# Optimization experiments

Hardware: AMD Instinct MI355X
Metric: run time of the kernel (lower is better)

The kernel has to match this reference:

```python
import jax, jax.numpy as jnp
import numpy as np

B, N, D = 4, 2048, 1024
H = 8
DK = D // H            # 128, head qk dim (pre feature map)
DV = D // H            # 128, head v dim
DF = 2 * DK            # 256, hedgehog feature dim
CHUNK = 64
RMS_EPS = 1e-5


def setup_inputs() -> dict:
    key = jax.random.key(0)
    ks = jax.random.split(key, 10)
    s = D ** -0.5
    x = jax.random.normal(ks[0], (B, N, D), dtype=jnp.float32)
    Wq = jax.random.normal(ks[1], (D, D), dtype=jnp.float32) * s
    Wk = jax.random.normal(ks[2], (D, D), dtype=jnp.float32) * s
    Wv = jax.random.normal(ks[3], (D, D), dtype=jnp.float32) * s
    Wo = jax.random.normal(ks[4], (D, D), dtype=jnp.float32) * s
    eye = jnp.eye(DK, dtype=jnp.float32)
    # Hedgehog maps are initialized as identity; add small noise to exercise math
    fmq_w = eye + 0.02 * jax.random.normal(ks[5], (DK, DK), dtype=jnp.float32)
    fmq_b = 0.02 * jax.random.normal(ks[6], (DK,), dtype=jnp.float32)
    fmk_w = eye + 0.02 * jax.random.normal(ks[7], (DK, DK), dtype=jnp.float32)
    fmk_b = 0.02 * jax.random.normal(ks[8], (DK,), dtype=jnp.float32)
    rms_w = 1.0 + 0.1 * jax.random.normal(ks[9], (DV,), dtype=jnp.float32)
    return {"x": x, "Wq": Wq, "Wk": Wk, "Wv": Wv, "Wo": Wo,
            "fmq_w": fmq_w, "fmq_b": fmq_b, "fmk_w": fmk_w, "fmk_b": fmk_b,
            "rms_w": rms_w}


def _hedgehog(x, w, b):
    # x: [B,H,N,DK]; Linear then concat(exp(y), exp(-y)) -> [B,H,N,2*DK]
    y = jnp.einsum('bhnd,ed->bhne', x, w) + b
    return jnp.concatenate([jnp.exp(y), jnp.exp(-y)], axis=-1)


def _fused_chunk_linear_attn(q, k, v):
    # Causal linear attention via chunked recurrence.
    # q,k: [B,H,N,DF]; v: [B,H,N,DV]; q already scaled.
    b, h, n, df = q.shape
    dv = v.shape[-1]
    nc = n // CHUNK
    def to_chunks(t):
        d = t.shape[-1]
        return t.reshape(b, h, nc, CHUNK, d).transpose(2, 0, 1, 3, 4)  # [Nc,B,H,C,d]
    qc, kc, vc = to_chunks(q), to_chunks(k), to_chunks(v)
    mask = jnp.tril(jnp.ones((CHUNK, CHUNK), dtype=bool))

    def step(S, inp):
        qi, ki, vi = inp                                   # [B,H,C,*]
        attn = jnp.einsum('bhcd,bhed->bhce', qi, ki)       # intra-chunk scores
        attn = jnp.where(mask, attn, 0.0)                  # causal (inclusive)
        intra = jnp.einsum('bhce,bhev->bhcv', attn, vi)
        inter = jnp.einsum('bhcd,bhdv->bhcv', qi, S)       # past-chunk state
        S = S + jnp.einsum('bhcd,bhcv->bhdv', ki, vi)
        return S, intra + inter

    S0 = jnp.zeros((b, h, df, dv), dtype=q.dtype)
    _, oc = jax.lax.scan(step, S0, (qc, kc, vc))           # oc: [Nc,B,H,C,DV]
    return oc.transpose(1, 2, 0, 3, 4).reshape(b, h, n, dv)


def reference(x, Wq, Wk, Wv, Wo, fmq_w, fmq_b, fmk_w, fmk_b, rms_w):
    b, n, d = x.shape
    split = lambda t: t.reshape(b, n, H, -1).transpose(0, 2, 1, 3)  # b h n d
    q = split(x @ Wq.T)
    k = split(x @ Wk.T)
    v = split(x @ Wv.T)
    q = _hedgehog(q, fmq_w, fmq_b)          # [B,H,N,DF]
    k = _hedgehog(k, fmk_w, fmk_b)
    scale = q.shape[-1] ** -0.5             # fla default: feat_dim**-0.5
    o = _fused_chunk_linear_attn(q * scale, k, v)
    # RMSNorm over head_v_dim
    o = o * jax.lax.rsqrt(jnp.mean(o * o, axis=-1, keepdims=True) + RMS_EPS) * rms_w
    o = o.transpose(0, 2, 1, 3).reshape(b, n, H * DV)
    return o @ Wo.T
```

## Files before the change

### kernel.cpp

```cpp
#include <hip/hip_runtime.h>
#include <cstdint>
#include <cstddef>

#define DEV __device__ __forceinline__

typedef __attribute__((ext_vector_type(8))) short   short8;
typedef __attribute__((ext_vector_type(4))) short   sshort4;
typedef __attribute__((ext_vector_type(8))) __bf16  bf16x8;
typedef __attribute__((ext_vector_type(4))) float   f32x4;

typedef void as1_void __attribute__((address_space(1)));
typedef void as3_void __attribute__((address_space(3)));

DEV short f2b(float f) {
  unsigned u = __float_as_uint(f);
  unsigned r = (u + 0x7fffu + ((u >> 16) & 1u)) >> 16;
  return (short)r;
}
DEV float b2f(short s) {
  return __uint_as_float(((unsigned)(unsigned short)s) << 16);
}

DEV void gload16(const void* g, void* l) {
  __builtin_amdgcn_global_load_lds((as1_void*)g, (as3_void*)l, 16, 0, 0);
}

DEV bf16x8 ld8(const short* p) { return *reinterpret_cast<const bf16x8*>(p); }

DEV f32x4 mfma16(bf16x8 a, bf16x8 b, f32x4 c) {
  return __builtin_amdgcn_mfma_f32_16x16x32_bf16(a, b, c, 0, 0, 0);
}

__global__ void prep_kernel(const float* __restrict__ x, const float* __restrict__ Wo,
                            const float* __restrict__ Wq, const float* __restrict__ Wk,
                            const float* __restrict__ Wv,
                            const float* __restrict__ fmq_w, const float* __restrict__ fmk_w,
                            short* __restrict__ x_b, short* __restrict__ Wo_b,
                            short* __restrict__ Wcat)
{
  const int blk = blockIdx.x;
  const int tid = threadIdx.x;
  if (blk < 5120) {
    const float* src;
    short* dst;
    int i;
    if (blk < 4096)      { src = x;  dst = x_b;            i = (blk * 256 + tid) * 8; }
    else if (blk < 4608) { src = Wo; dst = Wo_b;           i = ((blk - 4096) * 256 + tid) * 8; }
    else                 { src = Wv; dst = Wcat + 2097152; i = ((blk - 4608) * 256 + tid) * 8; }
    float4 a = *(const float4*)(src + i);
    float4 b = *(const float4*)(src + i + 4);
    short8 o;
    o[0] = f2b(a.x); o[1] = f2b(a.y); o[2] = f2b(a.z); o[3] = f2b(a.w);
    o[4] = f2b(b.x); o[5] = f2b(b.y); o[6] = f2b(b.z); o[7] = f2b(b.w);
    *(short8*)(dst + i) = o;
  } else {
    __shared__ float fm[16 * 128];
    const int eb = blk - 5120;
    const int sel = eb >> 6, h = (eb >> 3) & 7, eg = eb & 7;
    const float* W   = sel ? Wk : Wq;
    const float* fmw = sel ? fmk_w : fmq_w;
    const int e0 = eg * 16;
    for (int i = tid; i < 2048; i += 256) fm[i] = fmw[e0 * 128 + i];
    __syncthreads();
    float acc[16][4] = {};
    for (int d = 0; d < 128; d += 4) {
      f32x4 w0 = *(const f32x4*)(W + (size_t)(h * 128 + d + 0) * 1024 + tid * 4);
      f32x4 w1 = *(const f32x4*)(W + (size_t)(h * 128 + d + 1) * 1024 + tid * 4);
      f32x4 w2 = *(const f32x4*)(W + (size_t)(h * 128 + d + 2) * 1024 + tid * 4);
      f32x4 w3 = *(const f32x4*)(W + (size_t)(h * 128 + d + 3) * 1024 + tid * 4);
#pragma unroll
      for (int e = 0; e < 16; ++e) {
        f32x4 fv = *(const f32x4*)&fm[e * 128 + d];
#pragma unroll
        for (int c = 0; c < 4; ++c)
          acc[e][c] += fv[0] * w0[c] + fv[1] * w1[c] + fv[2] * w2[c] + fv[3] * w3[c];
      }
    }
#pragma unroll
    for (int e = 0; e < 16; ++e) {
      sshort4 o;
#pragma unroll
      for (int c = 0; c < 4; ++c) o[c] = f2b(acc[e][c]);
      *(sshort4*)(Wcat + (size_t)(sel * 1024 + h * 128 + e0 + e) * 1024 + tid * 4) = o;
    }
  }
}

template<int EPI>
__launch_bounds__(512, 2)
__global__ void gemm256(const short* __restrict__ A, const short* __restrict__ B,
                        const int K, const int N, float* __restrict__ C,
                        const float* __restrict__ qb, const float* __restrict__ kb,
                        short* __restrict__ qf, short* __restrict__ kf,
                        short* __restrict__ kfT, short* __restrict__ vT)
{
  __shared__ __align__(16) short lds[65536];
  float* ep = (float*)lds;

  const int tid = threadIdx.x;
  const int w = tid >> 6, l = tid & 63;
  const int wr = w >> 2, wc = w & 3;

  const int nbx = gridDim.x;
  const int orig = blockIdx.y * nbx + blockIdx.x;
  const int cpx = (nbx * gridDim.y) >> 3;
  const int wg = (orig & 7) * cpx + (orig >> 3);
  const int m0 = (wg / nbx) * 256, n0 = (wg % nbx) * 256;

  const int srow = tid >> 3;
  const int scol = ((tid & 7) ^ (srow & 7)) * 8;
  const int wbase = w * 8;

  f32x4 acc[8][4] = {};
  bf16x8 af[4][2];
  bf16x8 bg[2][2][2];

  auto STG = [&](const short* src, int g0, int p, int aoff, int R, int t) {
    gload16(src + (size_t)(g0 + R + srow) * K + t * 64 + scol,
            lds + p * 32768 + aoff + (R + wbase) * 64);
  };

#pragma unroll
  for (int R = 0; R < 256; R += 64) {
    STG(A, m0, 0, 0, R, 0);
    STG(B, n0, 0, 16384, R, 0);
    STG(A, m0, 1, 0, R, 1);
    STG(B, n0, 1, 16384, R, 1);
  }
  asm volatile("s_waitcnt vmcnt(0)" ::: "memory");
  __builtin_amdgcn_s_barrier();

#define PHASE(p, q, DOLDA, DOLDB, STAGES, TAIL) { \
    if (DOLDA) { \
      _Pragma("unroll") \
      for (int m = 0; m < 4; ++m) { \
        const int r = wr * 128 + ((q) >> 1) * 64 + m * 16 + (l & 15); \
        _Pragma("unroll") \
        for (int kk = 0; kk < 2; ++kk) \
          af[m][kk] = ld8(lds + (p) * 32768 + r * 64 + ((kk * 4 + (l >> 4)) ^ (r & 7)) * 8); \
      } \
    } \
    if (DOLDB) { \
      _Pragma("unroll") \
      for (int n = 0; n < 2; ++n) { \
        const int r = wc * 64 + ((q) & 1) * 32 + n * 16 + (l & 15); \
        _Pragma("unroll") \
        for (int kk = 0; kk < 2; ++kk) \
          bg[(q) & 1][n][kk] = ld8(lds + (p) * 32768 + 16384 + r * 64 + ((kk * 4 + (l >> 4)) ^ (r & 7)) * 8); \
      } \
    } \
    STAGES; \
    __builtin_amdgcn_s_barrier(); \
    asm volatile("s_waitcnt lgkmcnt(0)" ::: "memory"); \
    __builtin_amdgcn_sched_barrier(0); \
    __builtin_amdgcn_s_setprio(1); \
    _Pragma("unroll") \
    for (int m = 0; m < 4; ++m) \
      _Pragma("unroll") \
      for (int n = 0; n < 2; ++n) \
        _Pragma("unroll") \
        for (int kk = 0; kk < 2; ++kk) \
          acc[((q) >> 1) * 4 + m][((q) & 1) * 2 + n] = \
            mfma16(af[m][kk], bg[(q) & 1][n][kk], acc[((q) >> 1) * 4 + m][((q) & 1) * 2 + n]); \
    __builtin_amdgcn_s_setprio(0); \
    TAIL; \
    __builtin_amdgcn_s_barrier(); \
  }

  const int NI = K >> 7;
  for (int i = 0; i < NI; ++i) {
    const int t1 = 2 * i + 1, t2 = 2 * i + 2, t3 = 2 * i + 3;
    const bool sE = (i < NI - 1), sL = (i > 0);
    PHASE(0, 0, 1, 1, {
      if (sL) { STG(A, m0, 1, 0, 64, t1); STG(A, m0, 1, 0, 192, t1);
                STG(B, n0, 1, 16384, 0, t1); STG(B, n0, 1, 16384, 64, t1); } }, {});
    PHASE(0, 1, 0, 1, {
      if (sL) { STG(B, n0, 1, 16384, 128, t1); STG(B, n0, 1, 16384, 192, t1); } }, {});
    PHASE(0, 2, 1, 0, {
      if (sE) { STG(A, m0, 0, 0, 0, t2); STG(A, m0, 0, 0, 128, t2); } }, {});
    PHASE(0, 3, 0, 0, {}, {
      if (i == NI - 1) { asm volatile("s_waitcnt vmcnt(0)" ::: "memory"); }
      else             { asm volatile("s_waitcnt vmcnt(2)" ::: "memory"); } });
    PHASE(1, 0, 1, 1, {
      if (sE) { STG(A, m0, 0, 0, 64, t2); STG(A, m0, 0, 0, 192, t2); } }, {});
    PHASE(1, 1, 0, 1, {
      if (sE) { STG(B, n0, 0, 16384, 0, t2); STG(B, n0, 0, 16384, 64, t2); } }, {});
    PHASE(1, 2, 1, 0, {
      if (sE) { STG(B, n0, 0, 16384, 128, t2); STG(B, n0, 0, 16384, 192, t2); } }, {});
    PHASE(1, 3, 0, 0, {
      if (sE) { STG(A, m0, 1, 0, 0, t3); STG(A, m0, 1, 0, 128, t3); } }, {
      asm volatile("s_waitcnt vmcnt(2)" ::: "memory"); });
  }
#undef PHASE

  const int seg = (EPI == 1) ? (n0 >> 10) : 0;
  const int b = m0 >> 11, tok0 = m0 & 2047, c0 = tok0 >> 6;
  const int hbase = (n0 & 1023) >> 7;
  const int bh0 = b * 8 + hbase;

#pragma unroll
  for (int h = 0; h < 4; ++h) {
    __syncthreads();
    if (wr == (h >> 1)) {
      const int mbase = (h & 1) * 4;
#pragma unroll
      for (int n = 0; n < 4; ++n) {
        const int cl = wc * 64 + n * 16 + (l & 15);
        float bb = 0.f;
        if constexpr (EPI == 1) bb = (seg == 0) ? qb[cl & 127] : (seg == 1) ? kb[cl & 127] : 0.f;
#pragma unroll
        for (int m4 = 0; m4 < 4; ++m4)
#pragma unroll
          for (int r = 0; r < 4; ++r) {
            const int rl = m4 * 16 + (l >> 4) * 4 + r;
            ep[rl * 264 + (cl ^ ((rl & 3) << 2))] = acc[mbase + m4][n][r] + bb;
          }
      }
    }
    __syncthreads();

    if constexpr (EPI == 0) {
#pragma unroll
      for (int it = 0; it < 8; ++it) {
        const int tl = it * 8 + (tid >> 6);
        const int cc4 = (tid & 63) * 4;
        f32x4 v4 = *(const f32x4*)&ep[tl * 264 + (cc4 ^ ((tl & 3) << 2))];
        *(f32x4*)(C + (size_t)(m0 + h * 64 + tl) * N + n0 + cc4) = v4;
      }
    } else {
      const int cc = c0 + h;
      if (seg <= 1) {
        short* dst = (seg == 0) ? qf : kf;
        const float sc = (seg == 0) ? 0.0625f : 1.0f;
#pragma unroll
        for (int it = 0; it < 8; ++it) {
          const int tl = it * 8 + (tid >> 6);
          const int cc4 = (tid & 63) * 4;
          f32x4 y4 = *(const f32x4*)&ep[tl * 264 + (cc4 ^ ((tl & 3) << 2))];
          sshort4 sp, sm;
#pragma unroll
          for (int j = 0; j < 4; ++j) {
            sp[j] = f2b(__expf(y4[j]) * sc);
            sm[j] = f2b(__expf(-y4[j]) * sc);
          }
          const int hh = cc4 >> 7, e = cc4 & 127;
          short* rowp = dst + ((size_t)(bh0 + hh) * 2048 + tok0 + h * 64 + tl) * 256;
          *(sshort4*)(rowp + e)       = sp;
          *(sshort4*)(rowp + 128 + e) = sm;
        }
        if (seg == 1) {
#pragma unroll
          for (int p2 = 0; p2 < 8; ++p2) {
            const int idx = p2 * 512 + tid;
            const int er = idx >> 3, oct = (idx & 7) * 8;
            const int hh = er >> 8, rr = er & 255, e = rr & 127, sg = rr >> 7;
            const int cgc = hh * 128 + e;
            short8 o;
#pragma unroll
            for (int ii = 0; ii < 8; ++ii) {
              float y = ep[(oct + ii) * 264 + (cgc ^ (((oct + ii) & 3) << 2))];
              o[ii] = f2b(__expf(sg ? -y : y));
            }
            *(short8*)(kfT + ((size_t)(bh0 + hh) * 32 + cc) * 16384 + (size_t)rr * 64 + oct) = o;
          }
        }
      } else {
#pragma unroll
        for (int p2 = 0; p2 < 4; ++p2) {
          const int idx = p2 * 512 + tid;
          const int er = idx >> 3, oct = (idx & 7) * 8;
          const int hh = er >> 7, vv = er & 127;
          short8 o;
#pragma unroll
          for (int ii = 0; ii < 8; ++ii)
            o[ii] = f2b(ep[(oct + ii) * 264 + (er ^ (((oct + ii) & 3) << 2))]);
          *(short8*)(vT + ((size_t)(bh0 + hh) * 32 + cc) * 8192 + (size_t)vv * 64 + oct) = o;
        }
      }
    }
  }
}

__launch_bounds__(256, 3)
__global__ void passA_kernel(const short* __restrict__ kfT, const short* __restrict__ vT,
                             short* __restrict__ GT)
{
  const int bhc = blockIdx.x;
  const int tid = threadIdx.x, w = tid >> 6, l = tid & 63;
  __shared__ __align__(16) short skT[256 * 64];
  __shared__ __align__(16) short svt[128 * 64];
  const short* kg = kfT + (size_t)bhc * 256 * 64;
  const short* vg = vT  + (size_t)bhc * 128 * 64;
  short* G = GT + (size_t)bhc * 128 * 256;
  const int sr8 = l >> 3, sl8 = ((l & 7) ^ sr8) * 8;

#pragma unroll
  for (int j = 0; j < 8; ++j) {
    const int seg = w * 8 + j;
    gload16(kg + (size_t)(seg * 8 + sr8) * 64 + sl8, skT + seg * 512);
  }
#pragma unroll
  for (int j = 0; j < 4; ++j) {
    const int seg = w * 4 + j;
    gload16(vg + (size_t)(seg * 8 + sr8) * 64 + sl8, svt + seg * 512);
  }
  __syncthreads();

#pragma unroll
  for (int mi = 0; mi < 2; ++mi) {
    const int v0 = w * 32 + mi * 16;
    bf16x8 a[2];
#pragma unroll
    for (int ks = 0; ks < 2; ++ks)
      a[ks] = ld8(svt + (v0 + (l & 15)) * 64 + ((ks * 4 + (l >> 4)) ^ (l & 7)) * 8);
    f32x4 acc[16] = {};
#pragma unroll
    for (int nt = 0; nt < 16; ++nt)
#pragma unroll
      for (int ks = 0; ks < 2; ++ks) {
        bf16x8 b = ld8(skT + (nt * 16 + (l & 15)) * 64 + ((ks * 4 + (l >> 4)) ^ (l & 7)) * 8);
        acc[nt] = mfma16(a[ks], b, acc[nt]);
      }
#pragma unroll
    for (int nt = 0; nt < 16; ++nt)
#pragma unroll
      for (int r = 0; r < 4; ++r)
        G[(v0 + (l >> 4) * 4 + r) * 256 + nt * 16 + (l & 15)] = f2b(acc[nt][r]);
  }
}

__global__ void prefix_kernel(short* __restrict__ GT) {
  const int bh = blockIdx.x >> 4, slab = blockIdx.x & 15;
  short* base = GT + (size_t)bh * 32 * 32768 + slab * 2048 + threadIdx.x * 8;
  float acc[8] = {};
  short8 g = *(const short8*)base;
  for (int c = 0; c < 32; ++c) {
    short* p = base + (size_t)c * 32768;
    short8 gn = {};
    if (c < 31) gn = *(const short8*)(p + 32768);
    short8 s;
#pragma unroll
    for (int j = 0; j < 8; ++j) s[j] = f2b(acc[j]);
    *(short8*)p = s;
#pragma unroll
    for (int j = 0; j < 8; ++j) acc[j] += b2f(g[j]);
    g = gn;
  }
}

__launch_bounds__(256, 3)
__global__ void passC_kernel(const short* __restrict__ qf, const short* __restrict__ kf,
                             const short* __restrict__ vT, const short* __restrict__ ST,
                             const float* __restrict__ rms_w, short* __restrict__ o_n)
{
  const int bhc = blockIdx.x, bh = bhc >> 5, c = bhc & 31;
  const int tid = threadIdx.x, w = tid >> 6, l = tid & 63;
  __shared__ __align__(16) short bufA[64 * 256];
  __shared__ __align__(16) short bufV[64 * 64];
  __shared__ __align__(16) short attn[64 * 72];
  const short* qg = qf + ((size_t)bh * 2048 + c * 64) * 256;
  const short* kg = kf + ((size_t)bh * 2048 + c * 64) * 256;
  const short* vg = vT + (size_t)bhc * 128 * 64;
  const short* sg = ST + (size_t)bhc * 128 * 256;
  const int r0 = w * 16;
  const int sr8 = l >> 3, sl8 = ((l & 7) ^ sr8) * 8;
  const int l5 = l >> 5, s32 = l & 31;

#pragma unroll
  for (int j = 0; j < 8; ++j) {
    const int seg = w * 8 + j;
    const int row = seg * 2 + l5;
    gload16(kg + (size_t)row * 256 + (s32 ^ (row & 7)) * 8, bufA + seg * 512);
  }
  bf16x8 qreg[8];
#pragma unroll
  for (int ks = 0; ks < 8; ++ks)
    qreg[ks] = ld8(qg + (size_t)(r0 + (l & 15)) * 256 + ks * 32 + (l >> 4) * 8);

  __syncthreads();
  f32x4 s[4] = {};
#pragma unroll
  for (int ks = 0; ks < 8; ++ks) {
    const int rs = ((ks * 4 + (l >> 4)) ^ (l & 7)) * 8;
#pragma unroll
    for (int nt = 0; nt < 4; ++nt)
      s[nt] = mfma16(qreg[ks], ld8(bufA + (nt * 16 + (l & 15)) * 256 + rs), s[nt]);
  }
#pragma unroll
  for (int nt = 0; nt < 4; ++nt)
#pragma unroll
    for (int r = 0; r < 4; ++r) {
      int rr = r0 + (l >> 4) * 4 + r;
      int tt = nt * 16 + (l & 15);
      attn[rr * 72 + tt] = (tt <= rr) ? f2b(s[nt][r]) : (short)0;
    }

  f32x4 o[8] = {};
#pragma unroll
  for (int h = 0; h < 2; ++h) {
    __syncthreads();
#pragma unroll
    for (int j = 0; j < 8; ++j) {
      const int seg = w * 8 + j;
      const int row = seg * 2 + l5;
      gload16(sg + (size_t)(h * 64 + row) * 256 + (s32 ^ (row & 7)) * 8, bufA + seg * 512);
    }
#pragma unroll
    for (int j = 0; j < 2; ++j) {
      const int seg = w * 2 + j;
      const int row = seg * 8 + sr8;
      gload16(vg + (size_t)(h * 64 + row) * 64 + sl8, bufV + seg * 512);
    }
    __syncthreads();
#pragma unroll
    for (int ks = 0; ks < 2; ++ks) {
      bf16x8 a = ld8(attn + (r0 + (l & 15)) * 72 + ks * 32 + (l >> 4) * 8);
      const int rs = ((ks * 4 + (l >> 4)) ^ (l & 7)) * 8;
#pragma unroll
      for (int nt = 0; nt < 4; ++nt)
        o[h * 4 + nt] = mfma16(a, ld8(bufV + (nt * 16 + (l & 15)) * 64 + rs), o[h * 4 + nt]);
    }
#pragma unroll
    for (int ks = 0; ks < 8; ++ks) {
      const int rs = ((ks * 4 + (l >> 4)) ^ (l & 7)) * 8;
#pragma unroll
      for (int nt = 0; nt < 4; ++nt)
        o[h * 4 + nt] = mfma16(qreg[ks], ld8(bufA + (nt * 16 + (l & 15)) * 256 + rs), o[h * 4 + nt]);
    }
  }

  const int b = bh >> 3, hh = bh & 7;
#pragma unroll
  for (int r = 0; r < 4; ++r) {
    float ss = 0.f;
#pragma unroll
    for (int nt = 0; nt < 8; ++nt) ss += o[nt][r] * o[nt][r];
    ss += __shfl_xor(ss, 1);
    ss += __shfl_xor(ss, 2);
    ss += __shfl_xor(ss, 4);
    ss += __shfl_xor(ss, 8);
    float sc = rsqrtf(ss * (1.0f / 128.0f) + 1e-5f);
    int tok = c * 64 + r0 + (l >> 4) * 4 + r;
    size_t ob = ((size_t)b * 2048 + tok) * 1024 + hh * 128;
#pragma unroll
    for (int nt = 0; nt < 8; ++nt) {
      int vcol = nt * 16 + (l & 15);
      o_n[ob + vcol] = f2b(o[nt][r] * sc * rms_w[vcol]);
    }
  }
}

extern "C" void kernel_launch(void* const* d_in, const int* in_sizes, int n_in,
                              void* d_out, int out_size, void* d_ws, size_t ws_size,
                              hipStream_t stream)
{
  const float* x     = (const float*)d_in[0];
  const float* Wq    = (const float*)d_in[1];
  const float* Wk    = (const float*)d_in[2];
  const float* Wv    = (const float*)d_in[3];
  const float* Wo    = (const float*)d_in[4];
  const float* fmq_w = (const float*)d_in[5];
  const float* fmq_b = (const float*)d_in[6];
  const float* fmk_w = (const float*)d_in[7];
  const float* fmk_b = (const float*)d_in[8];
  const float* rms_w = (const float*)d_in[9];
  float* out = (float*)d_out;

  char* ws = (char*)d_ws;
  short* x_b  = (short*)(ws);
  short* Wcat = (short*)(ws + 16777216);
  short* Wo_b = (short*)(ws + 23068672);
  short* qf   = (short*)(ws + 25165824);
  short* kf   = (short*)(ws + 58720256);
  short* kfT  = (short*)(ws + 92274688);
  short* vT   = (short*)(ws + 125829120);
  short* GT   = (short*)(ws + 142606336);
  short* o_n  = x_b;

  prep_kernel<<<5248, 256, 0, stream>>>(x, Wo, Wq, Wk, Wv, fmq_w, fmk_w,
                                        x_b, Wo_b, Wcat);
  gemm256<1><<<dim3(12, 32), 512, 0, stream>>>(x_b, Wcat, 1024, 3072, nullptr,
                                               fmq_b, fmk_b, qf, kf, kfT, vT);
  passA_kernel<<<1024, 256, 0, stream>>>(kfT, vT, GT);
  prefix_kernel<<<512, 256, 0, stream>>>(GT);
  passC_kernel<<<1024, 256, 0, stream>>>(qf, kf, vT, GT, rms_w, o_n);
  gemm256<0><<<dim3(4, 32), 512, 0, stream>>>(o_n, Wo_b, 1024, 1024, out,
                                              nullptr, nullptr, nullptr, nullptr,
                                              nullptr, nullptr);
}
```

Measured before the change: 355.3 us.

## Add dedicated 256x128-tile GEMM for output projection to double grid size

Replaces the generic 256x256-tile GEMM used for the Wo output projection with a specialized kernel using 256x128 tiles. The grid grows from 128 to 256 workgroups, so more of the GPU's compute units get work on the 8192x1024x1024 GEMM. The kernel also remaps workgroup IDs for locality, uses a phased double-buffered LDS pipeline with partial prefetch, and writes the output through a staged LDS epilogue. The trade-off is lower per-tile reuse of A and B data and extra code to maintain.

```diff
diff --git a/kernel.cpp b/kernel.cpp
--- a/kernel.cpp
+++ b/kernel.cpp
@@ -281,6 +281,125 @@
   }
 }
 
+__launch_bounds__(512, 2)
+__global__ void gemm_wo(const short* __restrict__ A, const short* __restrict__ B,
+                        float* __restrict__ C)
+{
+  const int K = 1024, N = 1024, NT = 16;
+  __shared__ __align__(16) short lds[49152];
+  float* ep = (float*)lds;
+
+  const int tid = threadIdx.x;
+  const int w = tid >> 6, l = tid & 63;
+  const int wr = w >> 1, wc = w & 1;
+
+  const int orig = blockIdx.y * 8 + blockIdx.x;
+  const int wg = (orig & 7) * 32 + (orig >> 3);
+  const int m0 = (wg >> 3) * 256, n0 = (wg & 7) * 128;
+
+  const int srow = tid >> 3;
+  const int scol = ((tid & 7) ^ (srow & 7)) * 8;
+  const int wbase = w * 8;
+
+  f32x4 acc[4][4] = {};
+  bf16x8 af[2][2];
+  bf16x8 bg[2][2][2];
+
+  auto STG = [&](const short* src, int g0, int p, int aoff, int R, int t) {
+    gload16(src + (size_t)(g0 + R + srow) * K + t * 64 + scol,
+            lds + p * 24576 + aoff + (R + wbase) * 64);
+  };
+
+#pragma unroll
+  for (int p = 0; p < 2; ++p) {
+    STG(A, m0, p, 0, 0, p);   STG(A, m0, p, 0, 64, p);
+    STG(A, m0, p, 0, 128, p); STG(A, m0, p, 0, 192, p);
+    STG(B, n0, p, 16384, 0, p); STG(B, n0, p, 16384, 64, p);
+  }
+  asm volatile("s_waitcnt vmcnt(0)" ::: "memory");
+  __builtin_amdgcn_s_barrier();
+
+#define PH(p, q, DOLDA, DOLDB, STAGES, TAIL) { \
+    if (DOLDA) { \
+      _Pragma("unroll") \
+      for (int m = 0; m < 2; ++m) { \
+        const int r = wr * 64 + ((q) >> 1) * 32 + m * 16 + (l & 15); \
+        _Pragma("unroll") \
+        for (int kk = 0; kk < 2; ++kk) \
+          af[m][kk] = ld8(lds + (p) * 24576 + r * 64 + ((kk * 4 + (l >> 4)) ^ (r & 7)) * 8); \
+      } \
+    } \
+    if (DOLDB) { \
+      _Pragma("unroll") \
+      for (int n = 0; n < 2; ++n) { \
+        const int r = wc * 64 + ((q) & 1) * 32 + n * 16 + (l & 15); \
+        _Pragma("unroll") \
+        for (int kk = 0; kk < 2; ++kk) \
+          bg[(q) & 1][n][kk] = ld8(lds + (p) * 24576 + 16384 + r * 64 + ((kk * 4 + (l >> 4)) ^ (r & 7)) * 8); \
+      } \
+    } \
+    STAGES; \
+    __builtin_amdgcn_s_barrier(); \
+    asm volatile("s_waitcnt lgkmcnt(0)" ::: "memory"); \
+    __builtin_amdgcn_sched_barrier(0); \
+    __builtin_amdgcn_s_setprio(1); \
+    _Pragma("unroll") \
+    for (int m = 0; m < 2; ++m) \
+      _Pragma("unroll") \
+      for (int n = 0; n < 2; ++n) \
+        _Pragma("unroll") \
+        for (int kk = 0; kk < 2; ++kk) \
+          acc[((q) >> 1) * 2 + m][((q) & 1) * 2 + n] = \
+            mfma16(af[m][kk], bg[(q) & 1][n][kk], acc[((q) >> 1) * 2 + m][((q) & 1) * 2 + n]); \
+    __builtin_amdgcn_s_setprio(0); \
+    TAIL; \
+    __builtin_amdgcn_s_barrier(); \
+  }
+
+  for (int i = 0; i < NT; ++i) {
+    const int p = i & 1;
+    const bool sM = (i >= 1) && (i + 1 < NT);
+    const bool sP = (i + 2 < NT);
+    PH(p, 0, 1, 1, {
+      if (sM) { STG(A, m0, p ^ 1, 0, 128, i + 1); STG(A, m0, p ^ 1, 0, 192, i + 1); } }, {});
+    PH(p, 1, 0, 1, {
+      if (sM) { STG(B, n0, p ^ 1, 16384, 0, i + 1); } }, {});
+    PH(p, 2, 1, 0, {
+      if (sM) { STG(B, n0, p ^ 1, 16384, 64, i + 1); } }, {});
+    PH(p, 3, 0, 0, {
+      if (sP) { STG(A, m0, p, 0, 0, i + 2); STG(A, m0, p, 0, 64, i + 2); } }, {
+      if (i < NT - 2)       { asm volatile("s_waitcnt vmcnt(2)" ::: "memory"); }
+      else if (i == NT - 2) { asm volatile("s_waitcnt vmcnt(0)" ::: "memory"); } });
+  }
+#undef PH
+
+#pragma unroll
+  for (int h = 0; h < 4; ++h) {
+    __syncthreads();
+    if (wr == h) {
+#pragma unroll
+      for (int ni = 0; ni < 4; ++ni) {
+        const int cl = wc * 64 + ni * 16 + (l & 15);
+#pragma unroll
+        for (int mi = 0; mi < 4; ++mi)
+#pragma unroll
+          for (int r = 0; r < 4; ++r) {
+            const int rl = mi * 16 + (l >> 4) * 4 + r;
+            ep[rl * 132 + (cl ^ ((rl & 3) << 2))] = acc[mi][ni][r];
+          }
+      }
+    }
+    __syncthreads();
+#pragma unroll
+    for (int it = 0; it < 4; ++it) {
+      const int tl = it * 16 + (tid >> 5);
+      const int q = tid & 31;
+      f32x4 v4 = *(const f32x4*)&ep[tl * 132 + ((q * 4) ^ ((tl & 3) << 2))];
+      *(f32x4*)(C + (size_t)(m0 + h * 64 + tl) * N + n0 + q * 4) = v4;
+    }
+  }
+}
+
 __launch_bounds__(256, 3)
 __global__ void passA_kernel(const short* __restrict__ kfT, const short* __restrict__ vT,
                              short* __restrict__ GT)
@@ -484,7 +603,5 @@
   passA_kernel<<<1024, 256, 0, stream>>>(kfT, vT, GT);
   prefix_kernel<<<512, 256, 0, stream>>>(GT);
   passC_kernel<<<1024, 256, 0, stream>>>(qf, kf, vT, GT, rms_w, o_n);
-  gemm256<0><<<dim3(4, 32), 512, 0, stream>>>(o_n, Wo_b, 1024, 1024, out,
-                                              nullptr, nullptr, nullptr, nullptr,
-                                              nullptr, nullptr);
-}
+  gemm_wo<<<dim3(8, 32), 512, 0, stream>>>(o_n, Wo_b, out);
+}
```

Result: faster. 345.4 us (-2.8%).
